# Performance work log

Measured on AMD Instinct MI355X. Metric: run time of the kernel, lower is better.

Reference implementation:

```python
import jax, jax.numpy as jnp
import numpy as np

N, E = 50000, 600000
D_IN, D_H, D_OUT = 512, 128, 1
BN_EPS = 1e-5


def setup_inputs() -> dict:
    key = jax.random.key(0)
    ks = jax.random.split(key, 16)
    s = 0.05
    inp = {
        "feature": jax.random.normal(ks[0], (N, D_IN), dtype=jnp.float32),
        "edge_index": jax.random.randint(ks[1], (2, E), 0, N, dtype=jnp.int32),
        "head_W": jax.random.normal(ks[2], (D_IN, D_H), dtype=jnp.float32) * s,
        "head_b": jnp.zeros((D_H,), dtype=jnp.float32),
        "gin_W1": jax.random.normal(ks[3], (D_H, D_H), dtype=jnp.float32) * s,
        "gin_b1": jnp.zeros((D_H,), dtype=jnp.float32),
        "lin_W1": jax.random.normal(ks[4], (D_H, D_H), dtype=jnp.float32) * s,
        "lin_b1": jnp.zeros((D_H,), dtype=jnp.float32),
        "gin_W2": jax.random.normal(ks[5], (D_H, D_H), dtype=jnp.float32) * s,
        "gin_b2": jnp.zeros((D_H,), dtype=jnp.float32),
        "lin_W2": jax.random.normal(ks[6], (D_H, D_H), dtype=jnp.float32) * s,
        "lin_b2": jnp.zeros((D_H,), dtype=jnp.float32),
        "tail_W": jax.random.normal(ks[7], (D_H, D_OUT), dtype=jnp.float32) * s,
        "tail_b": jnp.zeros((D_OUT,), dtype=jnp.float32),
        "bn_gamma": jnp.ones((D_OUT,), dtype=jnp.float32),
        "bn_beta": jnp.zeros((D_OUT,), dtype=jnp.float32),
    }
    return inp


def _gin_layer(x, src, dst, gin_W, gin_b, lin_W, lin_b):
    # PyG GINConv, eps=0: nn((1+eps)*x + sum_{j in N(i)} x_j)
    agg = jax.ops.segment_sum(x[src], dst, num_segments=N)  # [N, D_H]
    h = jax.nn.relu((x + agg) @ gin_W + gin_b)              # GIN MLP (dropout p=0)
    return h @ lin_W + lin_b                                # plain post-linear


def reference(feature, edge_index, head_W, head_b,
              gin_W1, gin_b1, lin_W1, lin_b1,
              gin_W2, gin_b2, lin_W2, lin_b2,
              tail_W, tail_b, bn_gamma, bn_beta):
    src, dst = edge_index[0], edge_index[1]
    x = jax.nn.relu(feature @ head_W + head_b)              # head block (dropout p=0)
    x = _gin_layer(x, src, dst, gin_W1, gin_b1, lin_W1, lin_b1)
    x = _gin_layer(x, src, dst, gin_W2, gin_b2, lin_W2, lin_b2)
    z = x @ tail_W + tail_b                                 # [N, 1]
    # BatchNorm1d in training mode: biased batch stats over the node dim
    mu = jnp.mean(z, axis=0, keepdims=True)
    var = jnp.mean((z - mu) ** 2, axis=0, keepdims=True)
    return (z - mu) * jax.lax.rsqrt(var + BN_EPS) * bn_gamma + bn_beta
```

## Files before the change

kernel.cpp:

```cpp
#include <hip/hip_runtime.h>

#define N_NODES 50000
#define N_EDGES 600000
#define DH 128
#define BN_EPS 1e-5f
#define SCAN_BLOCKS ((N_NODES + 255) / 256)
#define HEAD_GRID ((N_NODES + 63) / 64)

typedef __attribute__((ext_vector_type(8))) short bf16x8;
typedef __attribute__((ext_vector_type(4))) float f32x4;

__device__ inline unsigned short f2bf(float x) {
  unsigned u = __float_as_uint(x);
  return (unsigned short)((u + 0x7FFFu + ((u >> 16) & 1u)) >> 16);
}
__device__ inline float bf2f(unsigned short h) {
  return __uint_as_float(((unsigned)h) << 16);
}

__device__ inline void gl_lds16(const unsigned short* g, unsigned short* l) {
  __builtin_amdgcn_global_load_lds(
      (const __attribute__((address_space(1))) unsigned int*)g,
      (__attribute__((address_space(3))) unsigned int*)l, 16, 0, 0);
}

__global__ __launch_bounds__(256) void convert_W5_count(
    const float* __restrict__ hW, const float* __restrict__ g1,
    const float* __restrict__ l1, const float* __restrict__ g2,
    const float* __restrict__ l2,
    unsigned short* __restrict__ hH, unsigned short* __restrict__ hL,
    unsigned short* __restrict__ g1H, unsigned short* __restrict__ g1L,
    unsigned short* __restrict__ l1H, unsigned short* __restrict__ l1L,
    unsigned short* __restrict__ g2H, unsigned short* __restrict__ g2L,
    unsigned short* __restrict__ l2H, unsigned short* __restrict__ l2L,
    const int* __restrict__ eidx, int* __restrict__ cnt,
    unsigned* __restrict__ xb_dummy) {
  int b = blockIdx.x;
  if (b >= 512) {
    int e = (b - 512) * 256 + threadIdx.x;
    if (e < N_EDGES) atomicAdd(&cnt[eidx[N_EDGES + e]], 1);
    return;
  }
  if (b == 0 && threadIdx.x < 64) xb_dummy[threadIdx.x] = 0u;
  const float* W;
  unsigned short *hi, *lo;
  int idx;
  if (b < 256) {
    W = hW; hi = hH; lo = hL;
    idx = b * 256 + threadIdx.x;
  } else {
    int w = (b - 256) >> 6;
    idx = ((b - 256) & 63) * 256 + threadIdx.x;
    W = (w == 0) ? g1 : (w == 1) ? l1 : (w == 2) ? g2 : l2;
    hi = (w == 0) ? g1H : (w == 1) ? l1H : (w == 2) ? g2H : l2H;
    lo = (w == 0) ? g1L : (w == 1) ? l1L : (w == 2) ? g2L : l2L;
  }
  int k = idx >> 7;
  int n = idx & 127;
  float x = W[idx];
  unsigned short h = f2bf(x);
  unsigned short l = f2bf(x - bf2f(h));
  int kstep = k >> 5;
  int ctile = ((n >> 6) << 2) | (n & 3);
  int cs = (n >> 2) & 15;
  int lane = ((k >> 3) & 3) * 16 + cs;
  int j = k & 7;
  size_t off = ((size_t)(kstep * 8 + ctile) * 64 + lane) * 8 + j;
  hi[off] = h;
  lo[off] = l;
}

__global__ __launch_bounds__(256) void gemm_head_fill(
    const float* __restrict__ A,
    const unsigned short* __restrict__ Bh, const unsigned short* __restrict__ Bl,
    const float* __restrict__ bias,
    unsigned short* __restrict__ xb_out, int M,
    const int* __restrict__ eidx, const int* __restrict__ rs,
    int* __restrict__ cursor, int* __restrict__ esrc) {
  constexpr int K = 512;
  constexpr int KSTEPS = K / 64;
  constexpr int ASTR = 72;
  __shared__ __align__(16) unsigned short Ah[64 * ASTR];
  __shared__ __align__(16) unsigned short Bhs[2][4096];
  __shared__ __align__(16) unsigned short Bls[2][4096];

  if (blockIdx.x >= HEAD_GRID) {
    int e = (blockIdx.x - HEAD_GRID) * 256 + threadIdx.x;
    if (e < N_EDGES) {
      int d = eidx[N_EDGES + e];
      int p = atomicAdd(&cursor[d], 1);
      esrc[rs[d] + p] = eidx[e];
    }
    return;
  }

  const int tid = threadIdx.x;
  const int wave = tid >> 6;
  const int lane = tid & 63;
  const int m0 = blockIdx.x * 64;

  const int s_row = tid >> 2;
  const int s_grp = tid & 3;
  const int g_row = m0 + s_row;
  const int g_rowc = (g_row < M) ? g_row : (M - 1);
  const float* af = A + (size_t)g_rowc * K + s_grp * 16;

  const int rgrp = wave & 1;
  const int ch = wave >> 1;

  f32x4 acc[2][4];
#pragma unroll
  for (int r = 0; r < 2; ++r)
#pragma unroll
    for (int c = 0; c < 4; ++c) acc[r][c] = (f32x4){0.f, 0.f, 0.f, 0.f};

  for (int ks = 0; ks < KSTEPS; ++ks) {
    {
      float4 f0 = *(const float4*)(af + ks * 64);
      float4 f1 = *(const float4*)(af + ks * 64 + 4);
      float4 f2 = *(const float4*)(af + ks * 64 + 8);
      float4 f3 = *(const float4*)(af + ks * 64 + 12);
      ushort4 h0, h1, h2, h3;
      h0.x = f2bf(f0.x); h0.y = f2bf(f0.y); h0.z = f2bf(f0.z); h0.w = f2bf(f0.w);
      h1.x = f2bf(f1.x); h1.y = f2bf(f1.y); h1.z = f2bf(f1.z); h1.w = f2bf(f1.w);
      h2.x = f2bf(f2.x); h2.y = f2bf(f2.y); h2.z = f2bf(f2.z); h2.w = f2bf(f2.w);
      h3.x = f2bf(f3.x); h3.y = f2bf(f3.y); h3.z = f2bf(f3.z); h3.w = f2bf(f3.w);
      int base = s_row * ASTR + s_grp * 16;
      *(ushort4*)&Ah[base + 0] = h0;
      *(ushort4*)&Ah[base + 4] = h1;
      *(ushort4*)&Ah[base + 8] = h2;
      *(ushort4*)&Ah[base + 12] = h3;
    }
#pragma unroll
    for (int s = 0; s < 2; ++s) {
      const unsigned short* sh = Bh + (size_t)(2 * ks + s) * 4096 + wave * 1024;
      const unsigned short* sl = Bl + (size_t)(2 * ks + s) * 4096 + wave * 1024;
      gl_lds16(sh + lane * 8, &Bhs[s][wave * 1024]);
      gl_lds16(sh + 512 + lane * 8, &Bhs[s][wave * 1024 + 512]);
      gl_lds16(sl + lane * 8, &Bls[s][wave * 1024]);
      gl_lds16(sl + 512 + lane * 8, &Bls[s][wave * 1024 + 512]);
    }
    __syncthreads();

#pragma unroll
    for (int s = 0; s < 2; ++s) {
      bf16x8 a0 = *(const bf16x8*)&Ah[(rgrp * 32 + (lane & 15)) * ASTR + s * 32 + (lane >> 4) * 8];
      bf16x8 a1 = *(const bf16x8*)&Ah[(rgrp * 32 + 16 + (lane & 15)) * ASTR + s * 32 + (lane >> 4) * 8];
#pragma unroll
      for (int c = 0; c < 4; ++c) {
        int ct = ch * 4 + c;
        bf16x8 bh = *(const bf16x8*)&Bhs[s][(ct * 64 + lane) * 8];
        bf16x8 bl = *(const bf16x8*)&Bls[s][(ct * 64 + lane) * 8];
        acc[0][c] = __builtin_amdgcn_mfma_f32_16x16x32_bf16(a0, bh, acc[0][c], 0, 0, 0);
        acc[0][c] = __builtin_amdgcn_mfma_f32_16x16x32_bf16(a0, bl, acc[0][c], 0, 0, 0);
        acc[1][c] = __builtin_amdgcn_mfma_f32_16x16x32_bf16(a1, bh, acc[1][c], 0, 0, 0);
        acc[1][c] = __builtin_amdgcn_mfma_f32_16x16x32_bf16(a1, bl, acc[1][c], 0, 0, 0);
      }
    }
    __syncthreads();
  }

  const int coln = lane & 15;
  const int rown = (lane >> 4) * 4;
  const int colbase = ch * 64 + coln * 4;
  const float4 bv = *(const float4*)(bias + colbase);
#pragma unroll
  for (int r = 0; r < 2; ++r) {
#pragma unroll
    for (int reg = 0; reg < 4; ++reg) {
      int row = m0 + rgrp * 32 + r * 16 + rown + reg;
      if (row < M) {
        ushort4 hb;
        hb.x = f2bf(fmaxf(acc[r][0][reg] + bv.x, 0.f));
        hb.y = f2bf(fmaxf(acc[r][1][reg] + bv.y, 0.f));
        hb.z = f2bf(fmaxf(acc[r][2][reg] + bv.z, 0.f));
        hb.w = f2bf(fmaxf(acc[r][3][reg] + bv.w, 0.f));
        *(ushort4*)&xb_out[(size_t)row * DH + colbase] = hb;
      }
    }
  }
}

__global__ __launch_bounds__(256) void gemm_gin(
    const unsigned short* __restrict__ yb,
    const unsigned short* __restrict__ B1h, const unsigned short* __restrict__ B1l,
    const float* __restrict__ b1,
    const unsigned short* __restrict__ B2h, const unsigned short* __restrict__ B2l,
    const float* __restrict__ b2,
    unsigned short* __restrict__ xb_out, int M,
    const float* __restrict__ tw, const float* __restrict__ tb,
    float* __restrict__ z, float* __restrict__ red) {
  constexpr int K = 128;
  constexpr int KSTEPS = K / 32;
  constexpr int ASTR = 40;
  constexpr int HSTR = 136;
  __shared__ __align__(16) unsigned short Ah[64 * ASTR];
  __shared__ __align__(16) unsigned short Bhs[4096];
  __shared__ __align__(16) unsigned short Bls[4096];
  __shared__ __align__(16) unsigned short Hb[64 * HSTR];

  const int tid = threadIdx.x;
  const int wave = tid >> 6;
  const int lane = tid & 63;
  const int m0 = blockIdx.x * 64;

  const int s_row = tid >> 2;
  const int s_oct = tid & 3;
  const int g_row = m0 + s_row;
  const int g_rowc = (g_row < M) ? g_row : (M - 1);
  const unsigned short* ab = yb + (size_t)g_rowc * K + s_oct * 8;

  const int rgrp = wave & 1;
  const int ch = wave >> 1;
  const int coln = lane & 15;
  const int rown = (lane >> 4) * 4;
  const int colbase = ch * 64 + coln * 4;

  auto issueB = [&](const unsigned short* Bh, const unsigned short* Bl, int ks) {
    const unsigned short* sh = Bh + (size_t)ks * 4096 + wave * 1024;
    const unsigned short* sl = Bl + (size_t)ks * 4096 + wave * 1024;
    gl_lds16(sh + lane * 8, &Bhs[wave * 1024]);
    gl_lds16(sh + 512 + lane * 8, &Bhs[wave * 1024 + 512]);
    gl_lds16(sl + lane * 8, &Bls[wave * 1024]);
    gl_lds16(sl + 512 + lane * 8, &Bls[wave * 1024 + 512]);
  };

  f32x4 acc[2][4];
#pragma unroll
  for (int r = 0; r < 2; ++r)
#pragma unroll
    for (int c = 0; c < 4; ++c) acc[r][c] = (f32x4){0.f, 0.f, 0.f, 0.f};

  for (int ks = 0; ks < KSTEPS; ++ks) {
    *(uint4*)&Ah[s_row * ASTR + s_oct * 8] = *(const uint4*)(ab + ks * 32);
    issueB(B1h, B1l, ks);
    __syncthreads();
    bf16x8 a0 = *(const bf16x8*)&Ah[(rgrp * 32 + (lane & 15)) * ASTR + (lane >> 4) * 8];
    bf16x8 a1 = *(const bf16x8*)&Ah[(rgrp * 32 + 16 + (lane & 15)) * ASTR + (lane >> 4) * 8];
#pragma unroll
    for (int c = 0; c < 4; ++c) {
      int ct = ch * 4 + c;
      bf16x8 bh = *(const bf16x8*)&Bhs[(ct * 64 + lane) * 8];
      bf16x8 bl = *(const bf16x8*)&Bls[(ct * 64 + lane) * 8];
      acc[0][c] = __builtin_amdgcn_mfma_f32_16x16x32_bf16(a0, bh, acc[0][c], 0, 0, 0);
      acc[0][c] = __builtin_amdgcn_mfma_f32_16x16x32_bf16(a0, bl, acc[0][c], 0, 0, 0);
      acc[1][c] = __builtin_amdgcn_mfma_f32_16x16x32_bf16(a1, bh, acc[1][c], 0, 0, 0);
      acc[1][c] = __builtin_amdgcn_mfma_f32_16x16x32_bf16(a1, bl, acc[1][c], 0, 0, 0);
    }
    __syncthreads();
  }

  {
    const float4 bv = *(const float4*)(b1 + colbase);
#pragma unroll
    for (int r = 0; r < 2; ++r) {
#pragma unroll
      for (int reg = 0; reg < 4; ++reg) {
        int lrow = rgrp * 32 + r * 16 + rown + reg;
        ushort4 hb;
        hb.x = f2bf(fmaxf(acc[r][0][reg] + bv.x, 0.f));
        hb.y = f2bf(fmaxf(acc[r][1][reg] + bv.y, 0.f));
        hb.z = f2bf(fmaxf(acc[r][2][reg] + bv.z, 0.f));
        hb.w = f2bf(fmaxf(acc[r][3][reg] + bv.w, 0.f));
        *(ushort4*)&Hb[lrow * HSTR + colbase] = hb;
      }
    }
#pragma unroll
    for (int r = 0; r < 2; ++r)
#pragma unroll
      for (int c = 0; c < 4; ++c) acc[r][c] = (f32x4){0.f, 0.f, 0.f, 0.f};
  }

  for (int ks = 0; ks < KSTEPS; ++ks) {
    issueB(B2h, B2l, ks);
    __syncthreads();
    bf16x8 a0 = *(const bf16x8*)&Hb[(rgrp * 32 + (lane & 15)) * HSTR + ks * 32 + (lane >> 4) * 8];
    bf16x8 a1 = *(const bf16x8*)&Hb[(rgrp * 32 + 16 + (lane & 15)) * HSTR + ks * 32 + (lane >> 4) * 8];
#pragma unroll
    for (int c = 0; c < 4; ++c) {
      int ct = ch * 4 + c;
      bf16x8 bh = *(const bf16x8*)&Bhs[(ct * 64 + lane) * 8];
      bf16x8 bl = *(const bf16x8*)&Bls[(ct * 64 + lane) * 8];
      acc[0][c] = __builtin_amdgcn_mfma_f32_16x16x32_bf16(a0, bh, acc[0][c], 0, 0, 0);
      acc[0][c] = __builtin_amdgcn_mfma_f32_16x16x32_bf16(a0, bl, acc[0][c], 0, 0, 0);
      acc[1][c] = __builtin_amdgcn_mfma_f32_16x16x32_bf16(a1, bh, acc[1][c], 0, 0, 0);
      acc[1][c] = __builtin_amdgcn_mfma_f32_16x16x32_bf16(a1, bl, acc[1][c], 0, 0, 0);
    }
    __syncthreads();
  }

  const float4 bv = *(const float4*)(b2 + colbase);

  if (tw == nullptr) {
#pragma unroll
    for (int r = 0; r < 2; ++r) {
#pragma unroll
      for (int reg = 0; reg < 4; ++reg) {
        int row = m0 + rgrp * 32 + r * 16 + rown + reg;
        if (row < M) {
          ushort4 hb;
          hb.x = f2bf(acc[r][0][reg] + bv.x);
          hb.y = f2bf(acc[r][1][reg] + bv.y);
          hb.z = f2bf(acc[r][2][reg] + bv.z);
          hb.w = f2bf(acc[r][3][reg] + bv.w);
          *(ushort4*)&xb_out[(size_t)row * DH + colbase] = hb;
        }
      }
    }
  } else {
    float* zpart = (float*)Hb;
    const float4 tw4 = *(const float4*)(tw + colbase);
#pragma unroll
    for (int r = 0; r < 2; ++r) {
#pragma unroll
      for (int reg = 0; reg < 4; ++reg) {
        int lrow = rgrp * 32 + r * 16 + rown + reg;
        float4 v;
        v.x = acc[r][0][reg] + bv.x;
        v.y = acc[r][1][reg] + bv.y;
        v.z = acc[r][2][reg] + bv.z;
        v.w = acc[r][3][reg] + bv.w;
        zpart[lrow * 33 + ch * 16 + coln] =
            v.x * tw4.x + v.y * tw4.y + v.z * tw4.z + v.w * tw4.w;
      }
    }
    __syncthreads();
    if (tid < 64) {
      int row = m0 + tid;
      float s = 0.f;
#pragma unroll
      for (int k = 0; k < 32; ++k) s += zpart[tid * 33 + k];
      float zv = s + tb[0];
      bool valid = row < M;
      if (valid) z[row] = zv;
      float a = valid ? zv : 0.f;
      float q = valid ? zv * zv : 0.f;
#pragma unroll
      for (int m = 32; m; m >>= 1) {
        a += __shfl_xor(a, m);
        q += __shfl_xor(q, m);
      }
      if (tid == 0) {
        atomicAdd(&red[0], a);
        atomicAdd(&red[1], q);
      }
    }
  }
}

__global__ __launch_bounds__(256) void scan_block(const int* __restrict__ cnt,
                                                  int* __restrict__ rs,
                                                  int* __restrict__ partials) {
  int t = threadIdx.x;
  int i = blockIdx.x * 256 + t;
  int v = (i < N_NODES) ? ((cnt[i] + 3) & ~3) : 0;
  __shared__ int s[256];
  s[t] = v;
  __syncthreads();
#pragma unroll
  for (int off = 1; off < 256; off <<= 1) {
    int add = (t >= off) ? s[t - off] : 0;
    __syncthreads();
    s[t] += add;
    __syncthreads();
  }
  if (i < N_NODES) rs[i] = s[t] - v;
  if (t == 255) partials[blockIdx.x] = s[255];
}

__global__ __launch_bounds__(256) void scan_partials(int* __restrict__ partials,
                                                     float* __restrict__ red) {
  int t = threadIdx.x;
  if (t == 0) { red[0] = 0.f; red[1] = 0.f; }
  int v = (t < SCAN_BLOCKS) ? partials[t] : 0;
  __shared__ int s[256];
  s[t] = v;
  __syncthreads();
#pragma unroll
  for (int off = 1; off < 256; off <<= 1) {
    int add = (t >= off) ? s[t - off] : 0;
    __syncthreads();
    s[t] += add;
    __syncthreads();
  }
  if (t < SCAN_BLOCKS) partials[t] = s[t] - v;
}

__global__ __launch_bounds__(256) void add_offsets_pad(
    int* __restrict__ rs, const int* __restrict__ partials,
    int* __restrict__ cnt, int* __restrict__ esrc) {
  int i = blockIdx.x * 256 + threadIdx.x;
  if (i >= N_NODES) return;
  int v = rs[i] + partials[blockIdx.x];
  rs[i] = v;
  int d = cnt[i];
  cnt[i] = 0;
  int pe = v + ((d + 3) & ~3);
  if (i == N_NODES - 1) rs[N_NODES] = pe;
  for (int k = v + d; k < pe; ++k) esrc[k] = N_NODES;
}

__global__ __launch_bounds__(256) void gin_aggregate_bf16(
    const unsigned short* __restrict__ xb,
    const int* __restrict__ rs, const int* __restrict__ esrc,
    unsigned* __restrict__ yb) {
  int node = blockIdx.x * 4 + (threadIdx.x >> 6);
  int lane = threadIdx.x & 63;
  if (node >= N_NODES) return;
  const unsigned* xb2 = (const unsigned*)xb;
  unsigned vs = xb2[(size_t)node * 64 + lane];
  float2 acc;
  acc.x = __uint_as_float(vs << 16);
  acc.y = __uint_as_float(vs & 0xFFFF0000u);
  int beg = rs[node];
  int end = rs[node + 1];
  int j = beg;
  for (; j + 8 <= end; j += 8) {
    int4 ia = *(const int4*)&esrc[j];
    int4 ib = *(const int4*)&esrc[j + 4];
    unsigned v0 = xb2[(size_t)ia.x * 64 + lane];
    unsigned v1 = xb2[(size_t)ia.y * 64 + lane];
    unsigned v2 = xb2[(size_t)ia.z * 64 + lane];
    unsigned v3 = xb2[(size_t)ia.w * 64 + lane];
    unsigned v4 = xb2[(size_t)ib.x * 64 + lane];
    unsigned v5 = xb2[(size_t)ib.y * 64 + lane];
    unsigned v6 = xb2[(size_t)ib.z * 64 + lane];
    unsigned v7 = xb2[(size_t)ib.w * 64 + lane];
    acc.x += ((__uint_as_float(v0 << 16) + __uint_as_float(v1 << 16)) +
              (__uint_as_float(v2 << 16) + __uint_as_float(v3 << 16))) +
             ((__uint_as_float(v4 << 16) + __uint_as_float(v5 << 16)) +
              (__uint_as_float(v6 << 16) + __uint_as_float(v7 << 16)));
    acc.y += ((__uint_as_float(v0 & 0xFFFF0000u) + __uint_as_float(v1 & 0xFFFF0000u)) +
              (__uint_as_float(v2 & 0xFFFF0000u) + __uint_as_float(v3 & 0xFFFF0000u))) +
             ((__uint_as_float(v4 & 0xFFFF0000u) + __uint_as_float(v5 & 0xFFFF0000u)) +
              (__uint_as_float(v6 & 0xFFFF0000u) + __uint_as_float(v7 & 0xFFFF0000u)));
  }
  if (j < end) {
    int4 ia = *(const int4*)&esrc[j];
    unsigned v0 = xb2[(size_t)ia.x * 64 + lane];
    unsigned v1 = xb2[(size_t)ia.y * 64 + lane];
    unsigned v2 = xb2[(size_t)ia.z * 64 + lane];
    unsigned v3 = xb2[(size_t)ia.w * 64 + lane];
    acc.x += (__uint_as_float(v0 << 16) + __uint_as_float(v1 << 16)) +
             (__uint_as_float(v2 << 16) + __uint_as_float(v3 << 16));
    acc.y += (__uint_as_float(v0 & 0xFFFF0000u) + __uint_as_float(v1 & 0xFFFF0000u)) +
             (__uint_as_float(v2 & 0xFFFF0000u) + __uint_as_float(v3 & 0xFFFF0000u));
  }
  yb[(size_t)node * 64 + lane] =
      (unsigned)f2bf(acc.x) | ((unsigned)f2bf(acc.y) << 16);
}

__global__ __launch_bounds__(256) void bn2(const float* __restrict__ z,
                                           const float* __restrict__ red,
                                           const float* __restrict__ gamma,
                                           const float* __restrict__ beta,
                                           float* __restrict__ out) {
  int i = blockIdx.x * 256 + threadIdx.x;
  if (i >= N_NODES) return;
  float mu = red[0] * (1.0f / N_NODES);
  float var = red[1] * (1.0f / N_NODES) - mu * mu;
  out[i] = (z[i] - mu) * rsqrtf(var + BN_EPS) * gamma[0] + beta[0];
}

extern "C" void kernel_launch(void* const* d_in, const int* in_sizes, int n_in,
                              void* d_out, int out_size, void* d_ws, size_t ws_size,
                              hipStream_t stream) {
  const float* feature = (const float*)d_in[0];
  const int* eidx = (const int*)d_in[1];
  const float* head_W = (const float*)d_in[2];
  const float* head_b = (const float*)d_in[3];
  const float* gin_W1 = (const float*)d_in[4];
  const float* gin_b1 = (const float*)d_in[5];
  const float* lin_W1 = (const float*)d_in[6];
  const float* lin_b1 = (const float*)d_in[7];
  const float* gin_W2 = (const float*)d_in[8];
  const float* gin_b2 = (const float*)d_in[9];
  const float* lin_W2 = (const float*)d_in[10];
  const float* lin_b2 = (const float*)d_in[11];
  const float* tail_W = (const float*)d_in[12];
  const float* tail_b = (const float*)d_in[13];
  const float* bn_gamma = (const float*)d_in[14];
  const float* bn_beta = (const float*)d_in[15];

  float* z = (float*)d_ws;
  float* red = z + N_NODES;
  int* row_start = (int*)(red + 2);
  int* cnt = row_start + (N_NODES + 1);
  int* partials = cnt + N_NODES;
  int* esrc = (int*)(((uintptr_t)(partials + 256) + 15) & ~(uintptr_t)15);
  unsigned short* wp =
      (unsigned short*)(((uintptr_t)(esrc + 760000) + 15) & ~(uintptr_t)15);
  unsigned short* hH = wp;
  unsigned short* hL = hH + 65536;
  unsigned short* g1H = hL + 65536;
  unsigned short* g1L = g1H + 16384;
  unsigned short* l1H = g1L + 16384;
  unsigned short* l1L = l1H + 16384;
  unsigned short* g2H = l1L + 16384;
  unsigned short* g2L = g2H + 16384;
  unsigned short* l2H = g2L + 16384;
  unsigned short* l2L = l2H + 16384;
  unsigned short* xb = l2L + 16384;
  unsigned short* yb = xb + (size_t)(N_NODES + 1) * DH;

  const int gin_grid = (N_NODES + 63) / 64;
  const int edge_grid = (N_EDGES + 255) / 256;
  const int agg_grid = (N_NODES + 3) / 4;

  hipMemsetAsync(cnt, 0, N_NODES * sizeof(int), stream);

  convert_W5_count<<<512 + edge_grid, 256, 0, stream>>>(
      head_W, gin_W1, lin_W1, gin_W2, lin_W2, hH, hL, g1H, g1L, l1H, l1L,
      g2H, g2L, l2H, l2L, eidx, cnt,
      (unsigned*)(xb + (size_t)N_NODES * DH));

  scan_block<<<SCAN_BLOCKS, 256, 0, stream>>>(cnt, row_start, partials);
  scan_partials<<<1, 256, 0, stream>>>(partials, red);
  add_offsets_pad<<<SCAN_BLOCKS, 256, 0, stream>>>(row_start, partials, cnt, esrc);

  gemm_head_fill<<<HEAD_GRID + edge_grid, 256, 0, stream>>>(
      feature, hH, hL, head_b, xb, N_NODES, eidx, row_start, cnt, esrc);

  gin_aggregate_bf16<<<agg_grid, 256, 0, stream>>>(xb, row_start, esrc,
                                                   (unsigned*)yb);
  gemm_gin<<<gin_grid, 256, 0, stream>>>(yb, g1H, g1L, gin_b1, l1H, l1L,
                                         lin_b1, xb, N_NODES,
                                         nullptr, nullptr, nullptr, nullptr);

  gin_aggregate_bf16<<<agg_grid, 256, 0, stream>>>(xb, row_start, esrc,
                                                   (unsigned*)yb);
  gemm_gin<<<gin_grid, 256, 0, stream>>>(yb, g2H, g2L, gin_b2, l2H, l2L,
                                         lin_b2, nullptr, N_NODES,
                                         tail_W, tail_b, z, red);

  bn2<<<(N_NODES + 255) / 256, 256, 0, stream>>>(z, red, bn_gamma, bn_beta, (float*)d_out);
}
```

Before: 364.3 us.

## Fuse GIN neighbor aggregation into GEMM kernel via LDS-staged aggregated tile

```diff
diff --git a/kernel.cpp b/kernel.cpp
--- a/kernel.cpp
+++ b/kernel.cpp
@@ -34,14 +34,17 @@
     unsigned short* __restrict__ g2H, unsigned short* __restrict__ g2L,
     unsigned short* __restrict__ l2H, unsigned short* __restrict__ l2L,
     const int* __restrict__ eidx, int* __restrict__ cnt,
-    unsigned* __restrict__ xb_dummy) {
+    unsigned* __restrict__ dummy0, unsigned* __restrict__ dummy1) {
   int b = blockIdx.x;
   if (b >= 512) {
     int e = (b - 512) * 256 + threadIdx.x;
     if (e < N_EDGES) atomicAdd(&cnt[eidx[N_EDGES + e]], 1);
     return;
   }
-  if (b == 0 && threadIdx.x < 64) xb_dummy[threadIdx.x] = 0u;
+  if (b == 0 && threadIdx.x < 64) {
+    dummy0[threadIdx.x] = 0u;
+    dummy1[threadIdx.x] = 0u;
+  }
   const float* W;
   unsigned short *hi, *lo;
   int idx;
@@ -181,8 +184,9 @@
   }
 }
 
-__global__ __launch_bounds__(256) void gemm_gin(
-    const unsigned short* __restrict__ yb,
+__global__ __launch_bounds__(256) void gemm_gin_fused(
+    const unsigned short* __restrict__ xb_in,
+    const int* __restrict__ rs, const int* __restrict__ esrc,
     const unsigned short* __restrict__ B1h, const unsigned short* __restrict__ B1l,
     const float* __restrict__ b1,
     const unsigned short* __restrict__ B2h, const unsigned short* __restrict__ B2l,
@@ -190,11 +194,8 @@
     unsigned short* __restrict__ xb_out, int M,
     const float* __restrict__ tw, const float* __restrict__ tb,
     float* __restrict__ z, float* __restrict__ red) {
-  constexpr int K = 128;
-  constexpr int KSTEPS = K / 32;
-  constexpr int ASTR = 40;
+  constexpr int KSTEPS = 4;
   constexpr int HSTR = 136;
-  __shared__ __align__(16) unsigned short Ah[64 * ASTR];
   __shared__ __align__(16) unsigned short Bhs[4096];
   __shared__ __align__(16) unsigned short Bls[4096];
   __shared__ __align__(16) unsigned short Hb[64 * HSTR];
@@ -203,12 +204,6 @@
   const int wave = tid >> 6;
   const int lane = tid & 63;
   const int m0 = blockIdx.x * 64;
-
-  const int s_row = tid >> 2;
-  const int s_oct = tid & 3;
-  const int g_row = m0 + s_row;
-  const int g_rowc = (g_row < M) ? g_row : (M - 1);
-  const unsigned short* ab = yb + (size_t)g_rowc * K + s_oct * 8;
 
   const int rgrp = wave & 1;
   const int ch = wave >> 1;
@@ -225,6 +220,57 @@
     gl_lds16(sl + 512 + lane * 8, &Bls[wave * 1024 + 512]);
   };
 
+  issueB(B1h, B1l, 0);
+
+  {
+    const unsigned* xb2 = (const unsigned*)xb_in;
+    for (int i = 0; i < 16; ++i) {
+      int lrow = wave * 16 + i;
+      int node = m0 + lrow;
+      float2 acc2 = {0.f, 0.f};
+      if (node < M) {
+        unsigned vs = xb2[(size_t)node * 64 + lane];
+        acc2.x = __uint_as_float(vs << 16);
+        acc2.y = __uint_as_float(vs & 0xFFFF0000u);
+        int j = rs[node];
+        int end = rs[node + 1];
+        for (; j + 8 <= end; j += 8) {
+          int4 ia = *(const int4*)&esrc[j];
+          int4 ib = *(const int4*)&esrc[j + 4];
+          unsigned v0 = xb2[(size_t)ia.x * 64 + lane];
+          unsigned v1 = xb2[(size_t)ia.y * 64 + lane];
+          unsigned v2 = xb2[(size_t)ia.z * 64 + lane];
+          unsigned v3 = xb2[(size_t)ia.w * 64 + lane];
+          unsigned v4 = xb2[(size_t)ib.x * 64 + lane];
+          unsigned v5 = xb2[(size_t)ib.y * 64 + lane];
+          unsigned v6 = xb2[(size_t)ib.z * 64 + lane];
+          unsigned v7 = xb2[(size_t)ib.w * 64 + lane];
+          acc2.x += ((__uint_as_float(v0 << 16) + __uint_as_float(v1 << 16)) +
+                     (__uint_as_float(v2 << 16) + __uint_as_float(v3 << 16))) +
+                    ((__uint_as_float(v4 << 16) + __uint_as_float(v5 << 16)) +
+                     (__uint_as_float(v6 << 16) + __uint_as_float(v7 << 16)));
+          acc2.y += ((__uint_as_float(v0 & 0xFFFF0000u) + __uint_as_float(v1 & 0xFFFF0000u)) +
+                     (__uint_as_float(v2 & 0xFFFF0000u) + __uint_as_float(v3 & 0xFFFF0000u))) +
+                    ((__uint_as_float(v4 & 0xFFFF0000u) + __uint_as_float(v5 & 0xFFFF0000u)) +
+                     (__uint_as_float(v6 & 0xFFFF0000u) + __uint_as_float(v7 & 0xFFFF0000u)));
+        }
+        if (j < end) {
+          int4 ia = *(const int4*)&esrc[j];
+          unsigned v0 = xb2[(size_t)ia.x * 64 + lane];
+          unsigned v1 = xb2[(size_t)ia.y * 64 + lane];
+          unsigned v2 = xb2[(size_t)ia.z * 64 + lane];
+          unsigned v3 = xb2[(size_t)ia.w * 64 + lane];
+          acc2.x += (__uint_as_float(v0 << 16) + __uint_as_float(v1 << 16)) +
+                    (__uint_as_float(v2 << 16) + __uint_as_float(v3 << 16));
+          acc2.y += (__uint_as_float(v0 & 0xFFFF0000u) + __uint_as_float(v1 & 0xFFFF0000u)) +
+                    (__uint_as_float(v2 & 0xFFFF0000u) + __uint_as_float(v3 & 0xFFFF0000u));
+        }
+      }
+      *(unsigned*)&Hb[lrow * HSTR + 2 * lane] =
+          (unsigned)f2bf(acc2.x) | ((unsigned)f2bf(acc2.y) << 16);
+    }
+  }
+
   f32x4 acc[2][4];
 #pragma unroll
   for (int r = 0; r < 2; ++r)
@@ -232,11 +278,10 @@
     for (int c = 0; c < 4; ++c) acc[r][c] = (f32x4){0.f, 0.f, 0.f, 0.f};
 
   for (int ks = 0; ks < KSTEPS; ++ks) {
-    *(uint4*)&Ah[s_row * ASTR + s_oct * 8] = *(const uint4*)(ab + ks * 32);
-    issueB(B1h, B1l, ks);
-    __syncthreads();
-    bf16x8 a0 = *(const bf16x8*)&Ah[(rgrp * 32 + (lane & 15)) * ASTR + (lane >> 4) * 8];
-    bf16x8 a1 = *(const bf16x8*)&Ah[(rgrp * 32 + 16 + (lane & 15)) * ASTR + (lane >> 4) * 8];
+    if (ks > 0) issueB(B1h, B1l, ks);
+    __syncthreads();
+    bf16x8 a0 = *(const bf16x8*)&Hb[(rgrp * 32 + (lane & 15)) * HSTR + ks * 32 + (lane >> 4) * 8];
+    bf16x8 a1 = *(const bf16x8*)&Hb[(rgrp * 32 + 16 + (lane & 15)) * HSTR + ks * 32 + (lane >> 4) * 8];
 #pragma unroll
     for (int c = 0; c < 4; ++c) {
       int ct = ch * 4 + c;
@@ -398,56 +443,6 @@
   int pe = v + ((d + 3) & ~3);
   if (i == N_NODES - 1) rs[N_NODES] = pe;
   for (int k = v + d; k < pe; ++k) esrc[k] = N_NODES;
-}
-
-__global__ __launch_bounds__(256) void gin_aggregate_bf16(
-    const unsigned short* __restrict__ xb,
-    const int* __restrict__ rs, const int* __restrict__ esrc,
-    unsigned* __restrict__ yb) {
-  int node = blockIdx.x * 4 + (threadIdx.x >> 6);
-  int lane = threadIdx.x & 63;
-  if (node >= N_NODES) return;
-  const unsigned* xb2 = (const unsigned*)xb;
-  unsigned vs = xb2[(size_t)node * 64 + lane];
-  float2 acc;
-  acc.x = __uint_as_float(vs << 16);
-  acc.y = __uint_as_float(vs & 0xFFFF0000u);
-  int beg = rs[node];
-  int end = rs[node + 1];
-  int j = beg;
-  for (; j + 8 <= end; j += 8) {
-    int4 ia = *(const int4*)&esrc[j];
-    int4 ib = *(const int4*)&esrc[j + 4];
-    unsigned v0 = xb2[(size_t)ia.x * 64 + lane];
-    unsigned v1 = xb2[(size_t)ia.y * 64 + lane];
-    unsigned v2 = xb2[(size_t)ia.z * 64 + lane];
-    unsigned v3 = xb2[(size_t)ia.w * 64 + lane];
-    unsigned v4 = xb2[(size_t)ib.x * 64 + lane];
-    unsigned v5 = xb2[(size_t)ib.y * 64 + lane];
-    unsigned v6 = xb2[(size_t)ib.z * 64 + lane];
-    unsigned v7 = xb2[(size_t)ib.w * 64 + lane];
-    acc.x += ((__uint_as_float(v0 << 16) + __uint_as_float(v1 << 16)) +
-              (__uint_as_float(v2 << 16) + __uint_as_float(v3 << 16))) +
-             ((__uint_as_float(v4 << 16) + __uint_as_float(v5 << 16)) +
-              (__uint_as_float(v6 << 16) + __uint_as_float(v7 << 16)));
-    acc.y += ((__uint_as_float(v0 & 0xFFFF0000u) + __uint_as_float(v1 & 0xFFFF0000u)) +
-              (__uint_as_float(v2 & 0xFFFF0000u) + __uint_as_float(v3 & 0xFFFF0000u))) +
-             ((__uint_as_float(v4 & 0xFFFF0000u) + __uint_as_float(v5 & 0xFFFF0000u)) +
-              (__uint_as_float(v6 & 0xFFFF0000u) + __uint_as_float(v7 & 0xFFFF0000u)));
-  }
-  if (j < end) {
-    int4 ia = *(const int4*)&esrc[j];
-    unsigned v0 = xb2[(size_t)ia.x * 64 + lane];
-    unsigned v1 = xb2[(size_t)ia.y * 64 + lane];
-    unsigned v2 = xb2[(size_t)ia.z * 64 + lane];
-    unsigned v3 = xb2[(size_t)ia.w * 64 + lane];
-    acc.x += (__uint_as_float(v0 << 16) + __uint_as_float(v1 << 16)) +
-             (__uint_as_float(v2 << 16) + __uint_as_float(v3 << 16));
-    acc.y += (__uint_as_float(v0 & 0xFFFF0000u) + __uint_as_float(v1 & 0xFFFF0000u)) +
-             (__uint_as_float(v2 & 0xFFFF0000u) + __uint_as_float(v3 & 0xFFFF0000u));
-  }
-  yb[(size_t)node * 64 + lane] =
-      (unsigned)f2bf(acc.x) | ((unsigned)f2bf(acc.y) << 16);
 }
 
 __global__ __launch_bounds__(256) void bn2(const float* __restrict__ z,
@@ -500,38 +495,34 @@
   unsigned short* g2L = g2H + 16384;
   unsigned short* l2H = g2L + 16384;
   unsigned short* l2L = l2H + 16384;
-  unsigned short* xb = l2L + 16384;
-  unsigned short* yb = xb + (size_t)(N_NODES + 1) * DH;
+  unsigned short* xb0 = l2L + 16384;
+  unsigned short* xb1 = xb0 + (size_t)(N_NODES + 1) * DH;
 
   const int gin_grid = (N_NODES + 63) / 64;
   const int edge_grid = (N_EDGES + 255) / 256;
-  const int agg_grid = (N_NODES + 3) / 4;
 
   hipMemsetAsync(cnt, 0, N_NODES * sizeof(int), stream);
 
   convert_W5_count<<<512 + edge_grid, 256, 0, stream>>>(
       head_W, gin_W1, lin_W1, gin_W2, lin_W2, hH, hL, g1H, g1L, l1H, l1L,
       g2H, g2L, l2H, l2L, eidx, cnt,
-      (unsigned*)(xb + (size_t)N_NODES * DH));
+      (unsigned*)(xb0 + (size_t)N_NODES * DH),
+      (unsigned*)(xb1 + (size_t)N_NODES * DH));
 
   scan_block<<<SCAN_BLOCKS, 256, 0, stream>>>(cnt, row_start, partials);
   scan_partials<<<1, 256, 0, stream>>>(partials, red);
   add_offsets_pad<<<SCAN_BLOCKS, 256, 0, stream>>>(row_start, partials, cnt, esrc);
 
   gemm_head_fill<<<HEAD_GRID + edge_grid, 256, 0, stream>>>(
-      feature, hH, hL, head_b, xb, N_NODES, eidx, row_start, cnt, esrc);
-
-  gin_aggregate_bf16<<<agg_grid, 256, 0, stream>>>(xb, row_start, esrc,
-                                                   (unsigned*)yb);
-  gemm_gin<<<gin_grid, 256, 0, stream>>>(yb, g1H, g1L, gin_b1, l1H, l1L,
-                                         lin_b1, xb, N_NODES,
-                                         nullptr, nullptr, nullptr, nullptr);
-
-  gin_aggregate_bf16<<<agg_grid, 256, 0, stream>>>(xb, row_start, esrc,
-                                                   (unsigned*)yb);
-  gemm_gin<<<gin_grid, 256, 0, stream>>>(yb, g2H, g2L, gin_b2, l2H, l2L,
-                                         lin_b2, nullptr, N_NODES,
-                                         tail_W, tail_b, z, red);
+      feature, hH, hL, head_b, xb0, N_NODES, eidx, row_start, cnt, esrc);
+
+  gemm_gin_fused<<<gin_grid, 256, 0, stream>>>(
+      xb0, row_start, esrc, g1H, g1L, gin_b1, l1H, l1L, lin_b1,
+      xb1, N_NODES, nullptr, nullptr, nullptr, nullptr);
+
+  gemm_gin_fused<<<gin_grid, 256, 0, stream>>>(
+      xb1, row_start, esrc, g2H, g2L, gin_b2, l2H, l2L, lin_b2,
+      nullptr, N_NODES, tail_W, tail_b, z, red);
 
   bn2<<<(N_NODES + 255) / 256, 256, 0, stream>>>(z, red, bn_gamma, bn_beta, (float*)d_out);
 }
```

Result: faster. 353.8 us (-2.9%).
